# Optimization experiments

Hardware: AMD Instinct MI355X
Metric: run time of the kernel (lower is better)

The kernel has to match this reference:

```python
import jax, jax.numpy as jnp
import numpy as np

KS, STRIDE, DIL = 5, 1, 1
PAD = (KS + (KS - 1) * (DIL - 1) - 1) // 2
EPS = 1e-5


def _unfold_t(x):
    # x: (N, C, T, V) -> (N, C, T_out, KS, V), zero-padded temporal windows
    N, C, T, V = x.shape
    xp = jnp.pad(x, ((0, 0), (0, 0), (PAD, PAD), (0, 0)))
    t_out = (T + 2 * PAD - DIL * (KS - 1) - 1) // STRIDE + 1
    idx = jnp.arange(t_out)[:, None] * STRIDE + jnp.arange(KS)[None, :] * DIL  # (T_out, KS)
    return xp[:, :, idx, :]


def _bn2d(x, g, b):
    # training-mode BatchNorm2d: biased batch stats over (N, T, V)
    mu = jnp.mean(x, axis=(0, 2, 3), keepdims=True)
    var = jnp.var(x, axis=(0, 2, 3), keepdims=True)
    xn = (x - mu) * jax.lax.rsqrt(var + EPS)
    return xn * g[None, :, None, None] + b[None, :, None, None]


def setup_inputs() -> dict:
    key = jax.random.key(0)
    ks = jax.random.split(key, 8)
    N, C, T, V = 64, 64, 128, 25
    R, O = 8, 128
    s = 0.05
    return {
        "x": jax.random.normal(ks[0], (N, C, T, V), jnp.float32),
        "Wv": jax.random.normal(ks[1], (R, C), jnp.float32) * s,
        "bv": jax.random.normal(ks[2], (R,), jnp.float32) * s,
        "Ww": jax.random.normal(ks[3], (KS * KS, KS), jnp.float32) * s,
        "bw": jax.random.normal(ks[4], (KS * KS,), jnp.float32) * s,
        "g_bn": jnp.ones((R,), jnp.float32),
        "b_bn": jnp.zeros((R,), jnp.float32),
        "Wr": jax.random.normal(ks[5], (R, C), jnp.float32) * s,
        "br": jax.random.normal(ks[6], (R,), jnp.float32) * s,
        "g_r": jnp.ones((R,), jnp.float32),
        "b_r": jnp.zeros((R,), jnp.float32),
        "Wo": jax.random.normal(ks[7], (O, R), jnp.float32) * s,
        "bo": jnp.zeros((O,), jnp.float32),
        "g_o": jnp.ones((O,), jnp.float32),
        "b_o": jnp.zeros((O,), jnp.float32),
    }


def reference(x, Wv, bv, Ww, bw, g_bn, b_bn, Wr, br, g_r, b_r, Wo, bo, g_o, b_o):
    N, C, T, V = x.shape
    # convV (1x1) then unfold both x and v
    v0 = jnp.einsum('rc,nctv->nrtv', Wv, x) + bv[None, :, None, None]
    xu = _unfold_t(x)      # (N, C, T, W, V)
    vu = _unfold_t(v0)     # (N, R, T, W, V)
    # mean over channels, move window dim to channel position for convW
    m = jnp.mean(xu, axis=1).transpose(0, 2, 1, 3)  # (N, W, T, V)
    w = jnp.einsum('ow,nwtv->notv', Ww, m) + bw[None, :, None, None]
    weights = jnp.tanh(w.reshape(N, KS, KS, T, V))  # (N, W, W, T, V)
    att = jnp.einsum('nwutv,nctuv->nctv', weights, vu)  # (N, R, T, V)
    # residual 1x1 conv + BN (in_channels != out_channels -> conv path)
    res = _bn2d(jnp.einsum('rc,nctv->nrtv', Wr, x) + br[None, :, None, None], g_r, b_r)
    h = _bn2d(att, g_bn, b_bn) + res
    h = jnp.where(h >= 0, h, 0.1 * h)  # LeakyReLU(0.1)
    out = _bn2d(jnp.einsum('or,nrtv->notv', Wo, h) + bo[None, :, None, None], g_o, b_o)
    return out
```

## Files before the change

kernel.cpp:

```cpp
#include <hip/hip_runtime.h>
#include <math.h>

#define TV 3200
#define NTV 204800
#define NB1 512
#define NB2 400
#define NB3 800
constexpr float EPSF = 1e-5f;

typedef float f2 __attribute__((ext_vector_type(2)));
typedef float f4 __attribute__((ext_vector_type(4)));

__device__ inline float fast_tanh(float x){
  float e = __expf(2.f*x);
  return 1.f - 2.f/(e + 1.f);
}

template<int NS>
__device__ inline void write_partials4(float (&vals)[NS], float* __restrict__ outp, int nb, float* lds){
  __syncthreads();
  int lane = threadIdx.x & 63, wid = threadIdx.x >> 6;
  #pragma unroll
  for (int s = 0; s < NS; ++s){
    float v = vals[s];
    #pragma unroll
    for (int o = 32; o > 0; o >>= 1) v += __shfl_down(v, o);
    if (lane == 0) lds[s*4 + wid] = v;
  }
  __syncthreads();
  if ((int)threadIdx.x < NS)
    outp[threadIdx.x*nb + blockIdx.x] = lds[threadIdx.x*4+0] + lds[threadIdx.x*4+1]
                                      + lds[threadIdx.x*4+2] + lds[threadIdx.x*4+3];
}

template<int NS>
__device__ inline void write_partials8(float (&vals)[NS], float* __restrict__ outp, int nb, float* lds){
  __syncthreads();
  int lane = threadIdx.x & 63, wid = threadIdx.x >> 6;
  #pragma unroll
  for (int s = 0; s < NS; ++s){
    float v = vals[s];
    #pragma unroll
    for (int o = 32; o > 0; o >>= 1) v += __shfl_down(v, o);
    if (lane == 0) lds[s*8 + wid] = v;
  }
  __syncthreads();
  if ((int)threadIdx.x < NS){
    float t = 0.f;
    #pragma unroll
    for (int w = 0; w < 8; ++w) t += lds[threadIdx.x*8 + w];
    outp[threadIdx.x*nb + blockIdx.x] = t;
  }
}

__global__ __launch_bounds__(512) void k_pw(
    const float* __restrict__ x,
    const float* __restrict__ Wv, const float* __restrict__ bv,
    const float* __restrict__ Wr, const float* __restrict__ br,
    const float* __restrict__ Ww, const float* __restrict__ bw,
    float* __restrict__ r0, float* __restrict__ att,
    float* __restrict__ pr, float* __restrict__ patt)
{
  __shared__ float sV[500*9];
  __shared__ float sS[500];
  __shared__ float sWvr[1024];
  __shared__ float sWw[125], sbw[25];
  __shared__ float red[16*8];
  const int tid = threadIdx.x;
  const int b = blockIdx.x, n = b >> 3, q = b & 7;
  const int t0 = q*16;
  for (int i2 = tid; i2 < 1024; i2 += 512){
    int c = i2 >> 4, k = i2 & 15;
    sWvr[i2] = (k < 8) ? Wv[k*64 + c] : Wr[(k-8)*64 + c];
  }
  if (tid < 125) sWw[tid] = Ww[tid];
  if (tid < 25)  sbw[tid] = bw[tid];
  __syncthreads();

  const int site = tid;
  const bool act = (site < 500);
  const bool val = act && (q > 0 || site >= 50) && (q < 7 || site < 450);
  const bool own = act && (site >= 50) && (site < 450);
  const float* xpn = x + (size_t)n*64*TV + (t0*25 - 50);
  const f4* sW4 = (const f4*)sWvr;

  float av[8]={0,0,0,0,0,0,0,0};
  float ar[8]={0,0,0,0,0,0,0,0};
  float ss = 0.f;
  if (val){
    #pragma unroll 8
    for (int c = 0; c < 64; ++c){
      float xv = __builtin_nontemporal_load(xpn + (size_t)c*TV + site);
      ss += xv;
      f4 wv0 = sW4[c*4+0], wv1 = sW4[c*4+1];
      f4 wr0 = sW4[c*4+2], wr1 = sW4[c*4+3];
      #pragma unroll
      for (int r = 0; r < 4; ++r){
        av[r]   = fmaf(wv0[r], xv, av[r]);
        av[4+r] = fmaf(wv1[r], xv, av[4+r]);
        ar[r]   = fmaf(wr0[r], xv, ar[r]);
        ar[4+r] = fmaf(wr1[r], xv, ar[4+r]);
      }
    }
  }
  if (act){
    sS[site] = ss * 0.015625f;
    #pragma unroll
    for (int r = 0; r < 8; ++r)
      sV[site*9+r] = val ? (av[r] + bv[r]) : 0.f;
  }
  const int gbase = t0*25 - 50 + site;
  float vals[16];
  {
    float rr[8];
    if (own){
      float* rp = r0 + (size_t)n*8*TV + gbase;
      #pragma unroll
      for (int r = 0; r < 8; ++r){
        rr[r] = ar[r] + br[r];
        rp[(size_t)r*TV] = rr[r];
      }
    }
    #pragma unroll
    for (int r = 0; r < 8; ++r){
      vals[r]   = own ? rr[r] : 0.f;
      vals[8+r] = own ? rr[r]*rr[r] : 0.f;
    }
  }
  write_partials8<16>(vals, pr, NB1, red);

  float at[8]={0,0,0,0,0,0,0,0};
  if (own){
    float m[5];
    #pragma unroll
    for (int k = 0; k < 5; ++k) m[k] = sS[site + (k-2)*25];
    float w2[5] = {0.f,0.f,0.f,0.f,0.f};
    #pragma unroll
    for (int w = 0; w < 5; ++w){
      #pragma unroll
      for (int u = 0; u < 5; ++u){
        int o = w*5 + u;
        float wo = sbw[o];
        #pragma unroll
        for (int k = 0; k < 5; ++k) wo = fmaf(sWw[o*5+k], m[k], wo);
        w2[u] += fast_tanh(wo);
      }
    }
    #pragma unroll
    for (int u = 0; u < 5; ++u){
      float wu = w2[u];
      int base = (site + (u-2)*25)*9;
      #pragma unroll
      for (int r = 0; r < 8; ++r) at[r] = fmaf(wu, sV[base + r], at[r]);
    }
    float* ap = att + (size_t)n*8*TV + gbase;
    #pragma unroll
    for (int r = 0; r < 8; ++r) ap[(size_t)r*TV] = at[r];
  }
  #pragma unroll
  for (int r = 0; r < 8; ++r){
    vals[r]   = own ? at[r] : 0.f;
    vals[8+r] = own ? at[r]*at[r] : 0.f;
  }
  write_partials8<16>(vals, patt, NB1, red);
}

__global__ __launch_bounds__(256) void k_h(
    const float* __restrict__ att, const float* __restrict__ r0,
    const float* __restrict__ pr, const float* __restrict__ patt,
    const float* __restrict__ g_bn, const float* __restrict__ b_bn,
    const float* __restrict__ g_r, const float* __restrict__ b_r,
    float* __restrict__ h, float* __restrict__ ph)
{
  __shared__ float red[44*4];
  __shared__ float sc[32];
  const int tid = threadIdx.x;
  {
    int g = tid >> 3, l8 = tid & 7;
    const float* src = (g < 16) ? (pr + g*NB1) : (patt + (g-16)*NB1);
    float sm = 0.f;
    for (int k2 = l8; k2 < NB1; k2 += 8) sm += src[k2];
    sm += __shfl_down(sm, 4, 8); sm += __shfl_down(sm, 2, 8); sm += __shfl_down(sm, 1, 8);
    if (l8 == 0) red[g] = sm;
  }
  __syncthreads();
  if (tid < 8){
    int r = tid;
    float mu_r  = red[r]    / (float)NTV;
    float var_r = red[8+r]  / (float)NTV - mu_r*mu_r;
    float ar_ = g_r[r] * rsqrtf(var_r + EPSF);
    sc[16+r] = ar_; sc[24+r] = b_r[r] - ar_*mu_r;
    float mu_a  = red[16+r] / (float)NTV;
    float var_a = red[24+r] / (float)NTV - mu_a*mu_a;
    float aa = g_bn[r] * rsqrtf(var_a + EPSF);
    sc[r] = aa; sc[8+r] = b_bn[r] - aa*mu_a;
  }
  __syncthreads();

  int p = blockIdx.x*256 + tid;
  int n = p / 1600, j = p - n*1600;
  const float* ap = att + (size_t)n*8*TV + 2*j;
  const float* rp = r0  + (size_t)n*8*TV + 2*j;
  float* hp = h + (size_t)n*8*TV + 2*j;
  float h0[8], h1[8];
  #pragma unroll
  for (int r = 0; r < 8; ++r){
    float ca = sc[r], cc = sc[8+r], cr = sc[16+r], cd = sc[24+r];
    f2 a = *(const f2*)(ap + (size_t)r*TV);
    f2 rr = *(const f2*)(rp + (size_t)r*TV);
    float z0 = ca*a.x + cc + cr*rr.x + cd;
    float z1 = ca*a.y + cc + cr*rr.y + cd;
    h0[r] = (z0 >= 0.f) ? z0 : 0.1f*z0;
    h1[r] = (z1 >= 0.f) ? z1 : 0.1f*z1;
    f2 hh; hh.x = h0[r]; hh.y = h1[r];
    *(f2*)(hp + (size_t)r*TV) = hh;
  }
  float vals[44];
  #pragma unroll
  for (int r = 0; r < 8; ++r) vals[r] = h0[r] + h1[r];
  int cnt = 8;
  #pragma unroll
  for (int r = 0; r < 8; ++r){
    #pragma unroll
    for (int r2 = r; r2 < 8; ++r2) vals[cnt++] = h0[r]*h0[r2] + h1[r]*h1[r2];
  }
  write_partials4<44>(vals, ph, NB2, red);
}

__global__ __launch_bounds__(256) void k_out(
    const float* __restrict__ h, const float* __restrict__ ph,
    const float* __restrict__ Wo, const float* __restrict__ bo,
    const float* __restrict__ g_o, const float* __restrict__ b_o,
    float* __restrict__ out)
{
  __shared__ float hstat[44];
  __shared__ float sW[1024], sB[128];
  const int tid = threadIdx.x;
  {
    int lane = tid & 63, wid = tid >> 6;
    for (int s2 = wid; s2 < 44; s2 += 4){
      float sm = 0.f;
      for (int k2 = lane; k2 < NB2; k2 += 64) sm += ph[s2*NB2 + k2];
      #pragma unroll
      for (int o = 32; o > 0; o >>= 1) sm += __shfl_down(sm, o);
      if (lane == 0) hstat[s2] = sm;
    }
  }
  __syncthreads();
  if (tid < 128){
    int o = tid;
    double muh[8];
    #pragma unroll
    for (int r = 0; r < 8; ++r) muh[r] = (double)hstat[r] / (double)NTV;
    double w[8];
    #pragma unroll
    for (int r = 0; r < 8; ++r) w[r] = (double)Wo[o*8+r];
    double bob = (double)bo[o];
    double mu = bob;
    #pragma unroll
    for (int r = 0; r < 8; ++r) mu += w[r]*muh[r];
    double t = 0.0;
    for (int r = 0; r < 8; ++r){
      for (int r2 = 0; r2 < 8; ++r2){
        int lo = (r < r2) ? r : r2, hi = (r < r2) ? r2 : r;
        int idx = 8 + lo*8 - (lo*(lo-1))/2 + (hi - lo);
        t += w[r]*w[r2]*((double)hstat[idx] / (double)NTV);
      }
    }
    double ey2 = t + 2.0*bob*(mu - bob) + bob*bob;
    double var = ey2 - mu*mu;
    double a = (double)g_o[o] / sqrt(var + (double)EPSF);
    #pragma unroll
    for (int r = 0; r < 8; ++r) sW[o*8+r] = (float)(a * w[r]);
    sB[o] = (float)(a * (bob - mu) + (double)b_o[o]);
  }
  __syncthreads();

  int p  = blockIdx.x*64 + (tid & 63);
  int oq = tid >> 6;
  int n = p / 800, j = p - n*800;
  const float* hp = h + (size_t)n*8*TV + 4*j;
  float hh[8][4];
  #pragma unroll
  for (int r = 0; r < 8; ++r){
    f4 v = *(const f4*)(hp + (size_t)r*TV);
    hh[r][0] = v[0]; hh[r][1] = v[1]; hh[r][2] = v[2]; hh[r][3] = v[3];
  }
  const f4* sW4 = (const f4*)sW;
  float* op = out + (size_t)n*128*TV + 4*j;
  #pragma unroll 4
  for (int oo = 0; oo < 32; ++oo){
    int o = oq*32 + oo;
    f4 w0 = sW4[o*2], w1 = sW4[o*2+1];
    float b = sB[o];
    f4 y; y.x = b; y.y = b; y.z = b; y.w = b;
    #pragma unroll
    for (int r = 0; r < 4; ++r){
      #pragma unroll
      for (int e = 0; e < 4; ++e){
        y[e] = fmaf(w0[r], hh[r][e], y[e]);
        y[e] = fmaf(w1[r], hh[4+r][e], y[e]);
      }
    }
    __builtin_nontemporal_store(y, (f4*)(op + (size_t)o*TV));
  }
}

extern "C" void kernel_launch(void* const* d_in, const int* in_sizes, int n_in,
                              void* d_out, int out_size, void* d_ws, size_t ws_size,
                              hipStream_t stream){
  const float* x    = (const float*)d_in[0];
  const float* Wv   = (const float*)d_in[1];
  const float* bv   = (const float*)d_in[2];
  const float* Ww   = (const float*)d_in[3];
  const float* bw   = (const float*)d_in[4];
  const float* g_bn = (const float*)d_in[5];
  const float* b_bn = (const float*)d_in[6];
  const float* Wr   = (const float*)d_in[7];
  const float* br   = (const float*)d_in[8];
  const float* g_r  = (const float*)d_in[9];
  const float* b_r  = (const float*)d_in[10];
  const float* Wo   = (const float*)d_in[11];
  const float* bo   = (const float*)d_in[12];
  const float* g_o  = (const float*)d_in[13];
  const float* b_o  = (const float*)d_in[14];

  float* ws = (float*)d_ws;
  size_t off = 0;
  float* r0   = ws + off; off += 1638400;
  float* att  = ws + off; off += 1638400;
  float* hbuf = ws + off; off += 1638400;
  float* pr   = ws + off; off += 16*NB1;
  float* patt = ws + off; off += 16*NB1;
  float* ph   = ws + off; off += 44*NB2;

  k_pw <<<NB1, 512, 0, stream>>>(x, Wv, bv, Wr, br, Ww, bw, r0, att, pr, patt);
  k_h  <<<NB2, 256, 0, stream>>>(att, r0, pr, patt, g_bn, b_bn, g_r, b_r, hbuf, ph);
  k_out<<<NB3, 256, 0, stream>>>(hbuf, ph, Wo, bo, g_o, b_o, (float*)d_out);
}
```

Before: 234.2 us.

## Recompute h in output kernel instead of materializing it, add fold kernel

Measured after the change: 244.6 us. 1.04x slower.

```diff
diff --git a/kernel.cpp b/kernel.cpp
--- a/kernel.cpp
+++ b/kernel.cpp
@@ -170,7 +170,7 @@
     const float* __restrict__ pr, const float* __restrict__ patt,
     const float* __restrict__ g_bn, const float* __restrict__ b_bn,
     const float* __restrict__ g_r, const float* __restrict__ b_r,
-    float* __restrict__ h, float* __restrict__ ph)
+    float* __restrict__ ph)
 {
   __shared__ float red[44*4];
   __shared__ float sc[32];
@@ -201,7 +201,6 @@
   int n = p / 1600, j = p - n*1600;
   const float* ap = att + (size_t)n*8*TV + 2*j;
   const float* rp = r0  + (size_t)n*8*TV + 2*j;
-  float* hp = h + (size_t)n*8*TV + 2*j;
   float h0[8], h1[8];
   #pragma unroll
   for (int r = 0; r < 8; ++r){
@@ -212,8 +211,6 @@
     float z1 = ca*a.y + cc + cr*rr.y + cd;
     h0[r] = (z0 >= 0.f) ? z0 : 0.1f*z0;
     h1[r] = (z1 >= 0.f) ? z1 : 0.1f*z1;
-    f2 hh; hh.x = h0[r]; hh.y = h1[r];
-    *(f2*)(hp + (size_t)r*TV) = hh;
   }
   float vals[44];
   #pragma unroll
@@ -227,14 +224,17 @@
   write_partials4<44>(vals, ph, NB2, red);
 }
 
-__global__ __launch_bounds__(256) void k_out(
-    const float* __restrict__ h, const float* __restrict__ ph,
+__global__ __launch_bounds__(256) void k_fold(
+    const float* __restrict__ ph,
+    const float* __restrict__ pr, const float* __restrict__ patt,
+    const float* __restrict__ g_bn, const float* __restrict__ b_bn,
+    const float* __restrict__ g_r, const float* __restrict__ b_r,
     const float* __restrict__ Wo, const float* __restrict__ bo,
     const float* __restrict__ g_o, const float* __restrict__ b_o,
-    float* __restrict__ out)
+    float* __restrict__ fold, float* __restrict__ bfold, float* __restrict__ gcoef)
 {
   __shared__ float hstat[44];
-  __shared__ float sW[1024], sB[128];
+  __shared__ float red[32];
   const int tid = threadIdx.x;
   {
     int lane = tid & 63, wid = tid >> 6;
@@ -246,7 +246,26 @@
       if (lane == 0) hstat[s2] = sm;
     }
   }
-  __syncthreads();
+  {
+    int g = tid >> 3, l8 = tid & 7;
+    const float* src = (g < 16) ? (pr + g*NB1) : (patt + (g-16)*NB1);
+    float sm = 0.f;
+    for (int k2 = l8; k2 < NB1; k2 += 8) sm += src[k2];
+    sm += __shfl_down(sm, 4, 8); sm += __shfl_down(sm, 2, 8); sm += __shfl_down(sm, 1, 8);
+    if (l8 == 0) red[g] = sm;
+  }
+  __syncthreads();
+  if (tid < 8){
+    int r = tid;
+    float mu_r  = red[r]    / (float)NTV;
+    float var_r = red[8+r]  / (float)NTV - mu_r*mu_r;
+    float ar_ = g_r[r] * rsqrtf(var_r + EPSF);
+    gcoef[16+r] = ar_; gcoef[24+r] = b_r[r] - ar_*mu_r;
+    float mu_a  = red[16+r] / (float)NTV;
+    float var_a = red[24+r] / (float)NTV - mu_a*mu_a;
+    float aa = g_bn[r] * rsqrtf(var_a + EPSF);
+    gcoef[r] = aa; gcoef[8+r] = b_bn[r] - aa*mu_a;
+  }
   if (tid < 128){
     int o = tid;
     double muh[8];
@@ -271,20 +290,40 @@
     double var = ey2 - mu*mu;
     double a = (double)g_o[o] / sqrt(var + (double)EPSF);
     #pragma unroll
-    for (int r = 0; r < 8; ++r) sW[o*8+r] = (float)(a * w[r]);
-    sB[o] = (float)(a * (bob - mu) + (double)b_o[o]);
-  }
+    for (int r = 0; r < 8; ++r) fold[o*8+r] = (float)(a * w[r]);
+    bfold[o] = (float)(a * (bob - mu) + (double)b_o[o]);
+  }
+}
+
+__global__ __launch_bounds__(256) void k_out(
+    const float* __restrict__ att, const float* __restrict__ r0,
+    const float* __restrict__ fold, const float* __restrict__ bfold,
+    const float* __restrict__ gcoef,
+    float* __restrict__ out)
+{
+  __shared__ float sW[1024], sB[128], sc[32];
+  const int tid = threadIdx.x;
+  for (int i = tid; i < 1024; i += 256) sW[i] = fold[i];
+  if (tid < 128) sB[tid] = bfold[tid];
+  if (tid < 32)  sc[tid] = gcoef[tid];
   __syncthreads();
 
   int p  = blockIdx.x*64 + (tid & 63);
   int oq = tid >> 6;
   int n = p / 800, j = p - n*800;
-  const float* hp = h + (size_t)n*8*TV + 4*j;
+  const float* ap = att + (size_t)n*8*TV + 4*j;
+  const float* rp = r0  + (size_t)n*8*TV + 4*j;
   float hh[8][4];
   #pragma unroll
   for (int r = 0; r < 8; ++r){
-    f4 v = *(const f4*)(hp + (size_t)r*TV);
-    hh[r][0] = v[0]; hh[r][1] = v[1]; hh[r][2] = v[2]; hh[r][3] = v[3];
+    float ca = sc[r], cr = sc[16+r], ccd = sc[8+r] + sc[24+r];
+    f4 a  = *(const f4*)(ap + (size_t)r*TV);
+    f4 rr = *(const f4*)(rp + (size_t)r*TV);
+    #pragma unroll
+    for (int e = 0; e < 4; ++e){
+      float z = fmaf(ca, a[e], fmaf(cr, rr[e], ccd));
+      hh[r][e] = (z >= 0.f) ? z : 0.1f*z;
+    }
   }
   const f4* sW4 = (const f4*)sW;
   float* op = out + (size_t)n*128*TV + 4*j;
@@ -327,14 +366,18 @@
 
   float* ws = (float*)d_ws;
   size_t off = 0;
-  float* r0   = ws + off; off += 1638400;
-  float* att  = ws + off; off += 1638400;
-  float* hbuf = ws + off; off += 1638400;
-  float* pr   = ws + off; off += 16*NB1;
-  float* patt = ws + off; off += 16*NB1;
-  float* ph   = ws + off; off += 44*NB2;
-
-  k_pw <<<NB1, 512, 0, stream>>>(x, Wv, bv, Wr, br, Ww, bw, r0, att, pr, patt);
-  k_h  <<<NB2, 256, 0, stream>>>(att, r0, pr, patt, g_bn, b_bn, g_r, b_r, hbuf, ph);
-  k_out<<<NB3, 256, 0, stream>>>(hbuf, ph, Wo, bo, g_o, b_o, (float*)d_out);
-}
+  float* r0    = ws + off; off += 1638400;
+  float* att   = ws + off; off += 1638400;
+  float* pr    = ws + off; off += 16*NB1;
+  float* patt  = ws + off; off += 16*NB1;
+  float* ph    = ws + off; off += 44*NB2;
+  float* fold  = ws + off; off += 1024;
+  float* bfold = ws + off; off += 128;
+  float* gcoef = ws + off; off += 32;
+
+  k_pw  <<<NB1, 512, 0, stream>>>(x, Wv, bv, Wr, br, Ww, bw, r0, att, pr, patt);
+  k_h   <<<NB2, 256, 0, stream>>>(att, r0, pr, patt, g_bn, b_bn, g_r, b_r, ph);
+  k_fold<<<1,   256, 0, stream>>>(ph, pr, patt, g_bn, b_bn, g_r, b_r, Wo, bo, g_o, b_o,
+                                  fold, bfold, gcoef);
+  k_out <<<NB3, 256, 0, stream>>>(att, r0, fold, bfold, gcoef, (float*)d_out);
+}
```
